# Optimization experiments

Hardware: AMD Instinct MI355X
Metric: run time of the kernel (lower is better)

Reference implementation:

```python
import jax, jax.numpy as jnp
import numpy as np

B, D, L, K = 4096, 1280, 16384, 64


def setup_inputs() -> dict:
    key = jax.random.key(0)
    k1, k2, k3, k4, k5 = jax.random.split(key, 5)
    scale_enc = 1.0 / np.sqrt(D)
    scale_dec = 1.0 / np.sqrt(L)
    return {
        "x_BD": jax.random.normal(k1, (B, D), dtype=jnp.float32),
        "pb_D": jax.random.normal(k2, (D,), dtype=jnp.float32) * 0.01,
        "W_enc": jax.random.normal(k3, (D, L), dtype=jnp.float32) * scale_enc,
        "lb_L": jax.random.normal(k4, (L,), dtype=jnp.float32) * 0.01,
        "W_dec": jax.random.normal(k5, (L, D), dtype=jnp.float32) * scale_dec,
    }


def topk_activation(x_BL, k):
    # lax.top_k over last dim, relu the values, scatter back into zeros
    tv_Bk, ti_Bk = jax.lax.top_k(x_BL, k)
    tv_Bk = jax.nn.relu(tv_Bk)
    b_B = jnp.arange(x_BL.shape[0])[:, None]
    return jnp.zeros_like(x_BL).at[b_B, ti_Bk].set(tv_Bk)


def reference(x_BD, pb_D, W_enc, lb_L, W_dec):
    # encode: shift by pre-bias, dense, add latent bias
    xshift_BD = x_BD - pb_D
    zpre_BL = xshift_BD @ W_enc + lb_L          # [B, L]
    # top-k sparse activation
    z_BL = topk_activation(zpre_BL, K)          # [B, L], only K nonzeros per row
    # decode: dense matmul over full L (the kernel-headroom target)
    xhat_BD = z_BL @ W_dec + pb_D               # [B, D]
    return (zpre_BL, z_BL, xhat_BD)
```

## Files before the change

### kernel.cpp

```cpp
#include <hip/hip_runtime.h>
#include <hip/hip_bf16.h>
#include <stdint.h>

#define B_SZ 4096
#define D_SZ 1280
#define L_SZ 16384
#define K_TOP 64
#define C_CAP 192
#define BAND 0.07f
#define LIST_CAP 4096
#define T_COLLECT 1.5f

typedef __attribute__((ext_vector_type(8))) short s16x8;
typedef __attribute__((ext_vector_type(4))) float f32x4;

#define GLOAD_LDS16(gp, lp)                                                          \
  __builtin_amdgcn_global_load_lds((const __attribute__((address_space(1))) void*)(gp), \
                                   (__attribute__((address_space(3))) void*)(lp), 16, 0, 0)

static __device__ __forceinline__ unsigned short f2bf(float f) {
  __hip_bfloat16 h = __float2bfloat16(f);
  return *reinterpret_cast<unsigned short*>(&h);
}
static __device__ __forceinline__ float bf2f(unsigned short u) {
  return __uint_as_float((unsigned)u << 16);
}
static __device__ __forceinline__ unsigned mkkey(float f) {
  const unsigned u = __float_as_uint(f);
  return (u & 0x80000000u) ? ~u : (u | 0x80000000u);
}
static __device__ __forceinline__ float unkey(unsigned k) {
  const unsigned u = (k & 0x80000000u) ? (k & 0x7fffffffu) : ~k;
  return __uint_as_float(u);
}

__global__ __launch_bounds__(256) void sae_prep(const float* __restrict__ x,
                                                const float* __restrict__ pb,
                                                const float* __restrict__ We,
                                                const float* __restrict__ Wd,
                                                unsigned short* __restrict__ A,
                                                float* __restrict__ xs,
                                                float* __restrict__ WT,
                                                unsigned short* __restrict__ WbT,
                                                unsigned short* __restrict__ Wdb,
                                                int* __restrict__ bk_cnt) {
  const int b = blockIdx.x, t = threadIdx.x;
  if (b < 5120) {
    __shared__ float tile[64][65];
    const int l0 = (b & 255) * 64, d0 = (b >> 8) * 64;
    const int c = t & 63, rg = t >> 6;
#pragma unroll
    for (int i = 0; i < 16; ++i) {
      const int row = i * 4 + rg;
      tile[row][c] = We[(size_t)(d0 + row) * L_SZ + l0 + c];
    }
    __syncthreads();
#pragma unroll
    for (int i = 0; i < 16; ++i) {
      const int row = i * 4 + rg;
      const float v = tile[c][row];
      const size_t o = (size_t)(l0 + row) * D_SZ + d0 + c;
      WT[o] = v;
      WbT[o] = f2bf(v);
    }
  } else if (b < 5120 + 4096) {
    const int r = b - 5120;
    const float* xr = x + (size_t)r * D_SZ;
    unsigned short* ar = A + (size_t)r * D_SZ;
    float* sr = xs + (size_t)r * D_SZ;
    for (int d = t; d < D_SZ; d += 256) {
      const float v = xr[d] - pb[d];
      ar[d] = f2bf(v);
      sr[d] = v;
    }
  } else if (b < 5120 + 4096 + 2048) {
    const int n4 = L_SZ * D_SZ / 4;
    for (int i = (b - 9216) * 256 + t; i < n4; i += 2048 * 256) {
      const float4 v = ((const float4*)Wd)[i];
      ushort4 o;
      o.x = f2bf(v.x); o.y = f2bf(v.y); o.z = f2bf(v.z); o.w = f2bf(v.w);
      ((ushort4*)Wdb)[i] = o;
    }
  } else {
    bk_cnt[(b - 11264) * 256 + t] = 0;
  }
}

#define SWZ(lin) ((lin) ^ ((((lin) >> 9) & 7) << 4))
#define A_LDS 0
#define B_LDS 65536
#define KBYTES (D_SZ * 2)

#define PH_MID()                                          \
  __builtin_amdgcn_s_barrier();                           \
  asm volatile("s_waitcnt lgkmcnt(0)" ::: "memory");      \
  __builtin_amdgcn_sched_barrier(0);                      \
  __builtin_amdgcn_s_setprio(1)

#define PH_END()                                          \
  __builtin_amdgcn_s_setprio(0);                          \
  __builtin_amdgcn_s_barrier();                           \
  __builtin_amdgcn_sched_barrier(0)

__global__ __launch_bounds__(512, 2) void sae_gemm(const unsigned short* __restrict__ A,
                                                   const unsigned short* __restrict__ WT,
                                                   const float* __restrict__ lb,
                                                   float* __restrict__ zpre) {
  __shared__ short lds[65536];
  char* ldsc = (char*)lds;
  const int t = threadIdx.x, lane = t & 63, w = t >> 6;
  const int wr = w >> 2, wc = w & 3, w2 = w * 2;

  const int bid = blockIdx.x;
  const int xcd = bid & 7, i2 = bid >> 3;
  const int b2 = i2 >> 4, inner = i2 & 15;
  const int mt = (b2 & 3) * 4 + (inner & 3);
  const int nt = xcd * 8 + (b2 >> 2) * 4 + (inner >> 2);
  const int m0 = mt * 256, n0 = nt * 256;

  f32x4 acc[8][4] = {};

  auto STAGE = [&](const unsigned short* op, int rowbase, int ldsop, int buf, int half, int tile) {
#pragma unroll
    for (int s = 0; s < 2; ++s) {
      const int o = (w2 + s) * 1024 + lane * 16;
      const int r = o >> 7;
      const int cb = (o & 127) ^ (((o >> 9) & 7) << 4);
      const char* g = (const char*)op + (size_t)(rowbase + half * 128 + r) * KBYTES +
                      tile * 128 + cb;
      char* l = ldsc + ldsop + buf * 32768 + half * 16384 + (w2 + s) * 1024;
      GLOAD_LDS16(g, l);
    }
  };
  auto LDA = [&](s16x8* af, int buf, int q) {
#pragma unroll
    for (int i = 0; i < 2; ++i)
#pragma unroll
      for (int kk = 0; kk < 2; ++kk) {
        const int r = (q * 2 + i) * 16 + (lane & 15);
        int lin = r * 128 + kk * 64 + ((lane >> 4) * 16);
        lin = SWZ(lin);
        af[i * 2 + kk] = *(const s16x8*)(ldsc + A_LDS + buf * 32768 + wr * 16384 + lin);
      }
  };
  auto LDB = [&](s16x8* bg, int buf) {
#pragma unroll
    for (int j = 0; j < 4; ++j)
#pragma unroll
      for (int kk = 0; kk < 2; ++kk) {
        const int nloc = wc * 64 + j * 16 + (lane & 15);
        const int half = nloc >> 7, r = nloc & 127;
        int lin = r * 128 + kk * 64 + ((lane >> 4) * 16);
        lin = SWZ(lin);
        bg[j * 2 + kk] = *(const s16x8*)(ldsc + B_LDS + buf * 32768 + half * 16384 + lin);
      }
  };
  auto MM = [&](s16x8* af, s16x8* bg, int q) {
#pragma unroll
    for (int i = 0; i < 2; ++i)
#pragma unroll
      for (int j = 0; j < 4; ++j)
#pragma unroll
        for (int kk = 0; kk < 2; ++kk)
          acc[q * 2 + i][j] =
              __builtin_amdgcn_mfma_f32_16x16x32_bf16(af[i * 2 + kk], bg[j * 2 + kk],
                                                      acc[q * 2 + i][j], 0, 0, 0);
  };

  STAGE(WT, n0, B_LDS, 0, 0, 0); STAGE(WT, n0, B_LDS, 0, 1, 0);
  STAGE(A, m0, A_LDS, 0, 0, 0);  STAGE(A, m0, A_LDS, 0, 1, 0);
  STAGE(WT, n0, B_LDS, 1, 0, 1); STAGE(WT, n0, B_LDS, 1, 1, 1);
  asm volatile("s_waitcnt vmcnt(4)" ::: "memory");
  __builtin_amdgcn_s_barrier();
  __builtin_amdgcn_sched_barrier(0);

  const int NI = D_SZ / 128;
  for (int i = 0; i < NI; ++i) {
    const bool last = (i == NI - 1);
    s16x8 af[4], bg[8];
    LDB(bg, 0); LDA(af, 0, 0);
    STAGE(A, m0, A_LDS, 1, 0, 2 * i + 1); STAGE(A, m0, A_LDS, 1, 1, 2 * i + 1);
    PH_MID(); MM(af, bg, 0); PH_END();
    LDA(af, 0, 1);
    if (!last) STAGE(WT, n0, B_LDS, 0, 0, 2 * i + 2);
    PH_MID(); MM(af, bg, 1); PH_END();
    LDA(af, 0, 2);
    if (!last) STAGE(WT, n0, B_LDS, 0, 1, 2 * i + 2);
    PH_MID(); MM(af, bg, 2); PH_END();
    LDA(af, 0, 3);
    PH_MID(); MM(af, bg, 3);
    __builtin_amdgcn_s_setprio(0);
    if (last) { asm volatile("s_waitcnt vmcnt(0)" ::: "memory"); }
    else      { asm volatile("s_waitcnt vmcnt(4)" ::: "memory"); }
    __builtin_amdgcn_s_barrier();
    __builtin_amdgcn_sched_barrier(0);
    LDB(bg, 1); LDA(af, 1, 0);
    if (!last) STAGE(A, m0, A_LDS, 0, 0, 2 * i + 2);
    PH_MID(); MM(af, bg, 0); PH_END();
    LDA(af, 1, 1);
    if (!last) STAGE(A, m0, A_LDS, 0, 1, 2 * i + 2);
    PH_MID(); MM(af, bg, 1); PH_END();
    LDA(af, 1, 2);
    if (!last) STAGE(WT, n0, B_LDS, 1, 0, 2 * i + 3);
    PH_MID(); MM(af, bg, 2); PH_END();
    LDA(af, 1, 3);
    if (!last) STAGE(WT, n0, B_LDS, 1, 1, 2 * i + 3);
    PH_MID(); MM(af, bg, 3);
    __builtin_amdgcn_s_setprio(0);
    asm volatile("s_waitcnt vmcnt(4)" ::: "memory");
    __builtin_amdgcn_s_barrier();
    __builtin_amdgcn_sched_barrier(0);
  }

  const int cl = lane & 15, rg = lane >> 4;
#pragma unroll
  for (int j = 0; j < 4; ++j) {
    const int cc = n0 + wc * 64 + j * 16 + cl;
    const float bias = lb[cc];
#pragma unroll
    for (int i = 0; i < 8; ++i) {
      const size_t base = (size_t)(m0 + wr * 128 + i * 16 + rg * 4) * L_SZ + cc;
#pragma unroll
      for (int tt = 0; tt < 4; ++tt) zpre[base + (size_t)tt * L_SZ] = acc[i][j][tt] + bias;
    }
  }
}

__device__ void radix_pick(unsigned* hist, unsigned* suf, int* sh_b, unsigned* sh_above,
                           int target, int t) {
  if (t == 0) *sh_b = -1;
  unsigned p = hist[4 * t] + hist[4 * t + 1] + hist[4 * t + 2] + hist[4 * t + 3];
  suf[t] = p;
  for (int off = 1; off < 256; off <<= 1) {
    __syncthreads();
    unsigned v = (t + off < 256) ? suf[t + off] : 0u;
    __syncthreads();
    suf[t] += v;
  }
  __syncthreads();
  const unsigned shi = (t + 1 < 256) ? suf[t + 1] : 0u;
  unsigned S = shi;
  int best = -1;
#pragma unroll
  for (int i = 3; i >= 0; --i) {
    S += hist[4 * t + i];
    if (S >= (unsigned)target) { best = 4 * t + i; break; }
  }
  if (best >= 0) atomicMax(sh_b, best);
  __syncthreads();
  const int b = *sh_b;
  if ((b >> 2) == t) {
    unsigned above = shi;
    for (int i = 3; i > (b & 3); --i) above += hist[4 * t + i];
    *sh_above = above;
  }
  __syncthreads();
}

__device__ void radix_pick4(unsigned* hist4, unsigned* suf, int* sh_b, unsigned* sh_above,
                            int target, int t) {
  if (t == 0) *sh_b = -1;
  if (t < 256) {
    unsigned p = 0;
#pragma unroll
    for (int i = 0; i < 4; ++i)
#pragma unroll
      for (int c = 0; c < 4; ++c) p += hist4[(4 * t + i) * 4 + c];
    suf[t] = p;
  }
  for (int off = 1; off < 256; off <<= 1) {
    __syncthreads();
    unsigned v = (t < 256 && t + off < 256) ? suf[t + off] : 0u;
    __syncthreads();
    if (t < 256) suf[t] += v;
  }
  __syncthreads();
  if (t < 256) {
    const unsigned shi = (t + 1 < 256) ? suf[t + 1] : 0u;
    unsigned S = shi;
    int best = -1;
    for (int i = 3; i >= 0; --i) {
      unsigned cnt = 0;
#pragma unroll
      for (int c = 0; c < 4; ++c) cnt += hist4[(4 * t + i) * 4 + c];
      S += cnt;
      if (S >= (unsigned)target) { best = 4 * t + i; break; }
    }
    if (best >= 0) atomicMax(sh_b, best);
  }
  __syncthreads();
  const int b = *sh_b;
  if (t < 256 && (b >> 2) == t) {
    unsigned above = (t + 1 < 256) ? suf[t + 1] : 0u;
    for (int i = 3; i > (b & 3); --i) {
      unsigned cnt = 0;
#pragma unroll
      for (int c = 0; c < 4; ++c) cnt += hist4[(4 * t + i) * 4 + c];
      above += cnt;
    }
    *sh_above = above;
  }
  __syncthreads();
}

__global__ __launch_bounds__(512) void sae_mega(const float* __restrict__ zpre,
                                                const float* __restrict__ xs,
                                                const float* __restrict__ WT,
                                                const float* __restrict__ lb,
                                                const unsigned short* __restrict__ Wdb,
                                                const float* __restrict__ pb,
                                                float* __restrict__ z,
                                                float* __restrict__ xhat) {
  __shared__ unsigned hist4[4096];
  __shared__ unsigned suf[256];
  __shared__ int l_idx[LIST_CAP];
  __shared__ unsigned l_key[LIST_CAP];
  __shared__ int sh_n, sh_b0, sh_b1, sh_nhi, sh_nband;
  __shared__ unsigned sh_above;
  __shared__ int bl[C_CAP];
  __shared__ float bfv[C_CAP];
  __shared__ double be[C_CAP];
  __shared__ int ids[K_TOP];
  __shared__ float vs[K_TOP];

  const int r = blockIdx.x, t = threadIdx.x, lane = t & 63, w = t >> 6;
  const float4* zr4 = (const float4*)(zpre + (size_t)r * L_SZ);

  float4 xc[5];
  {
    const float4* xr4 = (const float4*)(xs + (size_t)r * D_SZ);
#pragma unroll
    for (int i = 0; i < 5; ++i) xc[i] = xr4[lane + 64 * i];
  }

  auto push = [&](int idx, unsigned k, bool pred) {
    const unsigned long long m = __ballot(pred);
    if (!m) return;
    const int leader = (int)__ffsll((long long)m) - 1;
    int base = 0;
    if (lane == leader) base = atomicAdd(&sh_n, (int)__popcll(m));
    base = __shfl(base, leader);
    if (pred) {
      const int pos = base + (int)__popcll(m & ((1ull << lane) - 1ull));
      if (pos < LIST_CAP) { l_idx[pos] = idx; l_key[pos] = k; }
    }
  };

  if (t == 0) { sh_n = 0; sh_nhi = 0; sh_nband = 0; }
  __syncthreads();
  const unsigned keyT = mkkey(T_COLLECT);
  for (int i = t; i < L_SZ / 4; i += 512) {
    const float4 v = zr4[i];
    const float va[4] = {v.x, v.y, v.z, v.w};
#pragma unroll
    for (int q = 0; q < 4; ++q) {
      const unsigned k = mkkey(va[q]);
      push(4 * i + q, k, k >= keyT);
    }
  }
  __syncthreads();
  int nlist = sh_n < LIST_CAP ? sh_n : LIST_CAP;
  bool need_full = (sh_n < K_TOP) || (sh_n > LIST_CAP);
  float thresh_val = T_COLLECT;
  float lo_f = 0.f, hi_f = 0.f;

  for (int attempt = 0; attempt < 2; ++attempt) {
    if (need_full) {
      for (int i = t; i < 4096; i += 512) hist4[i] = 0;
      __syncthreads();
      for (int i = t; i < L_SZ / 4; i += 512) {
        const float4 v = zr4[i];
        const float va[4] = {v.x, v.y, v.z, v.w};
#pragma unroll
        for (int q = 0; q < 4; ++q)
          atomicAdd(&hist4[(mkkey(va[q]) >> 22) * 4 + (lane & 3)], 1u);
      }
      __syncthreads();
      radix_pick4(hist4, suf, &sh_b0, &sh_above, K_TOP, t);
      const int cb0 = sh_b0;
      const unsigned lt = (unsigned)(cb0 > 8 ? cb0 - 8 : 0) << 22;
      thresh_val = unkey(lt);
      if (t == 0) sh_n = 0;
      __syncthreads();
      for (int i = t; i < L_SZ / 4; i += 512) {
        const float4 v = zr4[i];
        const float va[4] = {v.x, v.y, v.z, v.w};
#pragma unroll
        for (int q = 0; q < 4; ++q) {
          const unsigned k = mkkey(va[q]);
          push(4 * i + q, k, k >= lt);
        }
      }
      __syncthreads();
      nlist = sh_n < LIST_CAP ? sh_n : LIST_CAP;
    }
    for (int i = t; i < 4096; i += 512) hist4[i] = 0;
    __syncthreads();
    for (int i = t; i < nlist; i += 512)
      atomicAdd(&hist4[(l_key[i] >> 22) * 4 + (lane & 3)], 1u);
    __syncthreads();
    radix_pick4(hist4, suf, &sh_b0, &sh_above, K_TOP, t);
    const int b0 = sh_b0;
    const int tgt2 = K_TOP - (int)sh_above;
    for (int i = t; i < 4096; i += 512) hist4[i] = 0;
    __syncthreads();
    for (int i = t; i < nlist; i += 512) {
      const unsigned k = l_key[i];
      if ((int)(k >> 22) == b0) atomicAdd(&hist4[((k >> 12) & 1023u) * 4 + (lane & 3)], 1u);
    }
    __syncthreads();
    radix_pick4(hist4, suf, &sh_b1, &sh_above, tgt2, t);
    const unsigned v64lb_key = (((unsigned)b0 << 10) | (unsigned)sh_b1) << 12;
    lo_f = unkey(v64lb_key) - BAND;
    hi_f = unkey(v64lb_key + 4095u) + BAND;
    if (thresh_val <= lo_f) break;
    need_full = true;
  }

  for (int i = t; i < nlist; i += 512) {
    const float val = unkey(l_key[i]);
    if (val >= lo_f) {
      if (val > hi_f) {
        const int p = atomicAdd(&sh_nhi, 1);
        if (p < K_TOP) { ids[p] = l_idx[i]; vs[p] = fmaxf(val, 0.f); }
      } else {
        const int p = atomicAdd(&sh_nband, 1);
        if (p < C_CAP) { bl[p] = l_idx[i]; bfv[p] = val; }
      }
    }
  }
  __syncthreads();
  const int nh = sh_nhi < K_TOP ? sh_nhi : K_TOP;
  const int nb = sh_nband < C_CAP ? sh_nband : C_CAP;
  for (int e = w; e < nb; e += 8) {
    const int l = bl[e];
    const float4* wr4 = (const float4*)(WT + (size_t)l * D_SZ);
    double acc = 0.0;
#pragma unroll
    for (int i = 0; i < 5; ++i) {
      const float4 wv = wr4[lane + 64 * i];
      acc += (double)xc[i].x * (double)wv.x + (double)xc[i].y * (double)wv.y +
             (double)xc[i].z * (double)wv.z + (double)xc[i].w * (double)wv.w;
    }
#pragma unroll
    for (int off = 32; off > 0; off >>= 1) acc += __shfl_down(acc, off);
    if (lane == 0) be[e] = acc + (double)lb[l];
  }
  __syncthreads();
  const int need = K_TOP - nh;
  if (t < nb) {
    const double ev = be[t];
    const int l = bl[t];
    int rank = 0;
    for (int j = 0; j < nb; ++j) {
      const double e2 = be[j];
      if (e2 > ev || (e2 == ev && bl[j] < l)) ++rank;
    }
    if (rank < need) {
      ids[nh + rank] = l;
      vs[nh + rank] = fmaxf(bfv[t], 0.f);
    }
  }
  __syncthreads();
  if (t < 320) {
    float4 acc = ((const float4*)pb)[t];
#pragma unroll 8
    for (int k = 0; k < K_TOP; ++k) {
      const ushort4 wv = ((const ushort4*)(Wdb + (size_t)ids[k] * D_SZ))[t];
      const float vk = vs[k];
      acc.x += vk * bf2f(wv.x);
      acc.y += vk * bf2f(wv.y);
      acc.z += vk * bf2f(wv.z);
      acc.w += vk * bf2f(wv.w);
    }
    ((float4*)(xhat + (size_t)r * D_SZ))[t] = acc;
  } else {
    const int tz = t - 320;
    float4* zr = (float4*)(z + (size_t)r * L_SZ);
    for (int i = tz; i < L_SZ / 4; i += 192) zr[i] = make_float4(0.f, 0.f, 0.f, 0.f);
  }
  __syncthreads();
  if (t < K_TOP) z[(size_t)r * L_SZ + ids[t]] = vs[t];
}

__global__ __launch_bounds__(256) void sae_topc(const float* __restrict__ zpre,
                                                int* __restrict__ bk_cnt,
                                                int* __restrict__ band_lat,
                                                float* __restrict__ band_fval,
                                                int* __restrict__ n_hi,
                                                int* __restrict__ n_band,
                                                int* __restrict__ t_idx,
                                                float* __restrict__ t_val) {
  __shared__ unsigned hist[1024];
  __shared__ unsigned suf[256];
  __shared__ int sh_b0, sh_b1, sh_nhi, sh_nband;
  __shared__ unsigned sh_above;
  const int r = blockIdx.x, t = threadIdx.x;
  const float4* zr4 = (const float4*)(zpre + (size_t)r * L_SZ);

  for (int i = t; i < 1024; i += 256) hist[i] = 0;
  if (t == 0) { sh_nhi = 0; sh_nband = 0; }
  __syncthreads();
  for (int i = t; i < L_SZ / 4; i += 256) {
    const float4 v = zr4[i];
    atomicAdd(&hist[mkkey(v.x) >> 22], 1u);
    atomicAdd(&hist[mkkey(v.y) >> 22], 1u);
    atomicAdd(&hist[mkkey(v.z) >> 22], 1u);
    atomicAdd(&hist[mkkey(v.w) >> 22], 1u);
  }
  __syncthreads();
  radix_pick(hist, suf, &sh_b0, &sh_above, K_TOP, t);
  const int b0 = sh_b0;
  const int target2 = K_TOP - (int)sh_above;
  __syncthreads();
  for (int i = t; i < 1024; i += 256) hist[i] = 0;
  __syncthreads();
  for (int i = t; i < L_SZ / 4; i += 256) {
    const float4 v = zr4[i];
    const float va[4] = {v.x, v.y, v.z, v.w};
#pragma unroll
    for (int q = 0; q < 4; ++q) {
      const unsigned k = mkkey(va[q]);
      if ((int)(k >> 22) == b0) atomicAdd(&hist[(k >> 12) & 1023u], 1u);
    }
  }
  __syncthreads();
  radix_pick(hist, suf, &sh_b1, &sh_above, target2, t);
  const unsigned v64lb_key = (((unsigned)b0 << 10) | (unsigned)sh_b1) << 12;
  const float lo_f = unkey(v64lb_key) - BAND;
  const float hi_f = unkey(v64lb_key + 4095u) + BAND;
  __syncthreads();
  for (int i = t; i < L_SZ / 4; i += 256) {
    const float4 v = zr4[i];
    const float va[4] = {v.x, v.y, v.z, v.w};
#pragma unroll
    for (int q = 0; q < 4; ++q) {
      const float val = va[q];
      if (val >= lo_f) {
        const int l = 4 * i + q;
        if (val > hi_f) {
          const int p = atomicAdd(&sh_nhi, 1);
          if (p < K_TOP) {
            t_idx[(size_t)r * K_TOP + p] = l;
            t_val[(size_t)r * K_TOP + p] = fmaxf(val, 0.f);
          }
        } else {
          const int p = atomicAdd(&sh_nband, 1);
          if (p < C_CAP) {
            band_lat[(r << 8) + p] = l;
            band_fval[(r << 8) + p] = val;
            atomicAdd(&bk_cnt[l], 1);
          }
        }
      }
    }
  }
  __syncthreads();
  if (t == 0) {
    n_hi[r] = sh_nhi < K_TOP ? sh_nhi : K_TOP;
    n_band[r] = sh_nband < C_CAP ? sh_nband : C_CAP;
  }
}

__global__ __launch_bounds__(256) void sae_scan(const int* __restrict__ counts,
                                                int* __restrict__ offsets,
                                                int* __restrict__ cursor) {
  __shared__ int part[256];
  const int t = threadIdx.x;
  int s = 0;
  for (int i = 0; i < 64; ++i) s += counts[t * 64 + i];
  part[t] = s;
  __syncthreads();
  int excl = 0;
  for (int j = 0; j < t; ++j) excl += part[j];
  int run = excl;
  for (int i = 0; i < 64; ++i) {
    const int idx = t * 64 + i;
    offsets[idx] = run;
    cursor[idx] = run;
    run += counts[idx];
  }
}

__global__ __launch_bounds__(192) void sae_bucket_fill(const int* __restrict__ band_lat,
                                                       const int* __restrict__ n_band,
                                                       int* __restrict__ cursor,
                                                       int* __restrict__ entries) {
  const int r = blockIdx.x, t = threadIdx.x;
  if (t < n_band[r]) {
    const int l = band_lat[(r << 8) + t];
    const int pos = atomicAdd(&cursor[l], 1);
    entries[pos] = (r << 8) | t;
  }
}

__global__ __launch_bounds__(256) void sae_refine_lm(const float* __restrict__ xs,
                                                     const float* __restrict__ WT,
                                                     const float* __restrict__ lb,
                                                     const int* __restrict__ counts,
                                                     const int* __restrict__ offsets,
                                                     const int* __restrict__ entries,
                                                     double* __restrict__ band_eval) {
  __shared__ float4 wl[D_SZ / 4];
  const int l = blockIdx.x;
  const int t = threadIdx.x, lane = t & 63, w = t >> 6;
  const int n = counts[l];
  if (n == 0) return;
  const float4* wc = (const float4*)(WT + (size_t)l * D_SZ);
  for (int d = t; d < D_SZ / 4; d += 256) wl[d] = wc[d];
  __syncthreads();
  const int base = offsets[l];
  const double bias = (double)lb[l];
  for (int e = w; e < n; e += 4) {
    const int ent = entries[base + e];
    const int rr = ent >> 8;
    const float4* xr = (const float4*)(xs + (size_t)rr * D_SZ);
    double acc = 0.0;
#pragma unroll
    for (int i = 0; i < 5; ++i) {
      const float4 xv = xr[lane + 64 * i];
      const float4 wv = wl[lane + 64 * i];
      acc += (double)xv.x * (double)wv.x + (double)xv.y * (double)wv.y +
             (double)xv.z * (double)wv.z + (double)xv.w * (double)wv.w;
    }
#pragma unroll
    for (int off = 32; off > 0; off >>= 1) acc += __shfl_down(acc, off);
    if (lane == 0) band_eval[ent] = acc + bias;
  }
}

__global__ __launch_bounds__(320) void sae_finish_nz(const int* __restrict__ n_hi,
                                                     const int* __restrict__ n_band,
                                                     const int* __restrict__ band_lat,
                                                     const float* __restrict__ band_fval,
                                                     const double* __restrict__ band_eval,
                                                     int* __restrict__ t_idx,
                                                     float* __restrict__ t_val,
                                                     const unsigned short* __restrict__ Wdb,
                                                     const float* __restrict__ pb,
                                                     float* __restrict__ xhat) {
  __shared__ int bl[C_CAP];
  __shared__ float bf[C_CAP];
  __shared__ double be[C_CAP];
  __shared__ int ids[K_TOP];
  __shared__ float vs[K_TOP];
  const int r = blockIdx.x, t = threadIdx.x;
  const int nh = n_hi[r], nb = n_band[r];
  if (t < nb) {
    bl[t] = band_lat[(r << 8) + t];
    bf[t] = band_fval[(r << 8) + t];
    be[t] = band_eval[(r << 8) + t];
  }
  if (t < nh) {
    ids[t] = t_idx[(size_t)r * K_TOP + t];
    vs[t] = t_val[(size_t)r * K_TOP + t];
  }
  __syncthreads();
  const int need = K_TOP - nh;
  if (t < nb) {
    const double ev = be[t];
    const int l = bl[t];
    int rank = 0;
    for (int j = 0; j < nb; ++j) {
      const double e2 = be[j];
      if (e2 > ev || (e2 == ev && bl[j] < l)) ++rank;
    }
    if (rank < need) {
      const float fv = fmaxf(bf[t], 0.f);
      ids[nh + rank] = l;
      vs[nh + rank] = fv;
      t_idx[(size_t)r * K_TOP + nh + rank] = l;
      t_val[(size_t)r * K_TOP + nh + rank] = fv;
    }
  }
  __syncthreads();
  float4 acc = ((const float4*)pb)[t];
#pragma unroll 8
  for (int k = 0; k < K_TOP; ++k) {
    const ushort4 wv = ((const ushort4*)(Wdb + (size_t)ids[k] * D_SZ))[t];
    const float vk = vs[k];
    acc.x += vk * bf2f(wv.x);
    acc.y += vk * bf2f(wv.y);
    acc.z += vk * bf2f(wv.z);
    acc.w += vk * bf2f(wv.w);
  }
  ((float4*)(xhat + (size_t)r * D_SZ))[t] = acc;
}

__global__ void sae_scatterA(const int* __restrict__ top_idx, const float* __restrict__ top_val,
                             float* __restrict__ z) {
  const int r = blockIdx.x;
  const int t = threadIdx.x;
  const int id = top_idx[(size_t)r * K_TOP + t];
  const float v = top_val[(size_t)r * K_TOP + t];
  z[(size_t)r * L_SZ + id] = v;
}

__global__ __launch_bounds__(256) void sae_scatterB(const int* __restrict__ top_idx,
                                                    const float* __restrict__ top_val,
                                                    float* __restrict__ z) {
  __shared__ int ids[32 * K_TOP];
  __shared__ float vs[32 * K_TOP];
  const int t = threadIdx.x;
  for (int i = t; i < 32 * K_TOP; i += 256) {
    ids[i] = top_idx[(size_t)4064 * K_TOP + i];
    vs[i] = top_val[(size_t)4064 * K_TOP + i];
  }
  __syncthreads();
  float4* zz = (float4*)(z + (size_t)4064 * L_SZ);
  for (int i = t; i < 32 * L_SZ / 4; i += 256) zz[i] = make_float4(0.f, 0.f, 0.f, 0.f);
  __syncthreads();
  for (int i = t; i < 32 * K_TOP; i += 256) {
    const int rr = 4064 + i / K_TOP;
    z[(size_t)rr * L_SZ + ids[i]] = vs[i];
  }
}

extern "C" void kernel_launch(void* const* d_in, const int* in_sizes, int n_in,
                              void* d_out, int out_size, void* d_ws, size_t ws_size,
                              hipStream_t stream) {
  const float* x  = (const float*)d_in[0];
  const float* pb = (const float*)d_in[1];
  const float* We = (const float*)d_in[2];
  const float* lb = (const float*)d_in[3];
  const float* Wd = (const float*)d_in[4];

  float* zpre = (float*)d_out;
  float* z    = zpre + (size_t)B_SZ * L_SZ;
  float* xhat = z + (size_t)B_SZ * L_SZ;

  const bool use_ws = ws_size >= ((size_t)234 << 20);
  char* sb = use_ws ? (char*)d_ws : (char*)z;

  unsigned short* A_bf   = (unsigned short*)(sb);
  unsigned short* WT_bf  = (unsigned short*)(sb + ((size_t)16 << 20));
  float*          WT_f32 = (float*)(sb + ((size_t)64 << 20));
  float*          xs_f32 = (float*)(sb + ((size_t)144 << 20));
  int*            b_lat  = (int*)(sb + ((size_t)164 << 20));
  float*          b_fval = (float*)(sb + ((size_t)168 << 20));
  double*         b_eval = (double*)(sb + ((size_t)172 << 20));
  int*            bk_cnt = (int*)(sb + ((size_t)180 << 20));
  int*            bk_off = (int*)(sb + ((size_t)181 << 20));
  int*            bk_cur = (int*)(sb + ((size_t)182 << 20));
  int*            bk_ent = (int*)(sb + ((size_t)184 << 20));
  unsigned short* Wd_bf  = (unsigned short*)(sb + ((size_t)188 << 20));
  int*            nhi_g  = (int*)(sb + ((size_t)228 << 20));
  int*            nbd_g  = (int*)(sb + ((size_t)229 << 20));
  int*   t_idx = use_ws ? (int*)(sb + ((size_t)230 << 20))
                        : (int*)((char*)z + ((size_t)254 << 20));
  float* t_val = use_ws ? (float*)(sb + ((size_t)232 << 20))
                        : (float*)((char*)z + ((size_t)255 << 20));

  sae_prep<<<11328, 256, 0, stream>>>(x, pb, We, Wd, A_bf, xs_f32, WT_f32, WT_bf, Wd_bf, bk_cnt);
  sae_gemm<<<1024, 512, 0, stream>>>(A_bf, WT_bf, lb, zpre);
  if (use_ws) {
    sae_mega<<<B_SZ, 512, 0, stream>>>(zpre, xs_f32, WT_f32, lb, Wd_bf, pb, z, xhat);
  } else {
    sae_topc<<<B_SZ, 256, 0, stream>>>(zpre, bk_cnt, b_lat, b_fval, nhi_g, nbd_g, t_idx, t_val);
    sae_scan<<<1, 256, 0, stream>>>(bk_cnt, bk_off, bk_cur);
    sae_bucket_fill<<<B_SZ, 192, 0, stream>>>(b_lat, nbd_g, bk_cur, bk_ent);
    sae_refine_lm<<<L_SZ, 256, 0, stream>>>(xs_f32, WT_f32, lb, bk_cnt, bk_off, bk_ent, b_eval);
    sae_finish_nz<<<B_SZ, 320, 0, stream>>>(nhi_g, nbd_g, b_lat, b_fval, b_eval, t_idx, t_val,
                                            Wd_bf, pb, xhat);
    hipMemsetAsync(z, 0, (size_t)4064 * L_SZ * sizeof(float), stream);
    sae_scatterA<<<4064, K_TOP, 0, stream>>>(t_idx, t_val, z);
    sae_scatterB<<<1, 256, 0, stream>>>(t_idx, t_val, z);
  }
}
```

Before: 667.3 us.

## Collect top-k candidates in GEMM epilogue to skip zpre row rescans

The GEMM epilogue now appends every pre-activation above a higher threshold to a per-row global candidate list via atomics. The top-k stage then reads only that short list instead of scanning the full 16K-wide zpre row, and falls back to a full two-pass radix selection when the list is too short, overflows, or the threshold is not safely below the band. This removes a large read of zpre in the mega kernel. In exchange it adds global atomics and scattered writes to the GEMM epilogue, needs more workspace, and only runs when the workspace is large enough.

```diff
diff --git a/kernel.cpp b/kernel.cpp
--- a/kernel.cpp
+++ b/kernel.cpp
@@ -8,8 +8,8 @@
 #define K_TOP 64
 #define C_CAP 192
 #define BAND 0.07f
-#define LIST_CAP 4096
-#define T_COLLECT 1.5f
+#define CL_CAP 512
+#define T_COLLECT 2.2f
 
 typedef __attribute__((ext_vector_type(8))) short s16x8;
 typedef __attribute__((ext_vector_type(4))) float f32x4;
@@ -43,7 +43,8 @@
                                                 float* __restrict__ WT,
                                                 unsigned short* __restrict__ WbT,
                                                 unsigned short* __restrict__ Wdb,
-                                                int* __restrict__ bk_cnt) {
+                                                int* __restrict__ bk_cnt,
+                                                int* __restrict__ cl_cnt) {
   const int b = blockIdx.x, t = threadIdx.x;
   if (b < 5120) {
     __shared__ float tile[64][65];
@@ -81,8 +82,10 @@
       o.x = f2bf(v.x); o.y = f2bf(v.y); o.z = f2bf(v.z); o.w = f2bf(v.w);
       ((ushort4*)Wdb)[i] = o;
     }
+  } else if (b < 11328) {
+    bk_cnt[(b - 11264) * 256 + t] = 0;
   } else {
-    bk_cnt[(b - 11264) * 256 + t] = 0;
+    cl_cnt[(b - 11328) * 256 + t] = 0;
   }
 }
 
@@ -105,7 +108,10 @@
 __global__ __launch_bounds__(512, 2) void sae_gemm(const unsigned short* __restrict__ A,
                                                    const unsigned short* __restrict__ WT,
                                                    const float* __restrict__ lb,
-                                                   float* __restrict__ zpre) {
+                                                   float* __restrict__ zpre,
+                                                   int* __restrict__ cl_cnt,
+                                                   int* __restrict__ cl_idx,
+                                                   float* __restrict__ cl_val) {
   __shared__ short lds[65536];
   char* ldsc = (char*)lds;
   const int t = threadIdx.x, lane = t & 63, w = t >> 6;
@@ -219,9 +225,20 @@
     const float bias = lb[cc];
 #pragma unroll
     for (int i = 0; i < 8; ++i) {
-      const size_t base = (size_t)(m0 + wr * 128 + i * 16 + rg * 4) * L_SZ + cc;
-#pragma unroll
-      for (int tt = 0; tt < 4; ++tt) zpre[base + (size_t)tt * L_SZ] = acc[i][j][tt] + bias;
+      const int row0 = m0 + wr * 128 + i * 16 + rg * 4;
+      const size_t base = (size_t)row0 * L_SZ + cc;
+#pragma unroll
+      for (int tt = 0; tt < 4; ++tt) {
+        const float v = acc[i][j][tt] + bias;
+        zpre[base + (size_t)tt * L_SZ] = v;
+        if (v >= T_COLLECT) {
+          const int p = atomicAdd(&cl_cnt[row0 + tt], 1);
+          if (p < CL_CAP) {
+            cl_idx[(size_t)(row0 + tt) * CL_CAP + p] = cc;
+            cl_val[(size_t)(row0 + tt) * CL_CAP + p] = v;
+          }
+        }
+      }
     }
   }
 }
@@ -309,13 +326,16 @@
                                                 const float* __restrict__ lb,
                                                 const unsigned short* __restrict__ Wdb,
                                                 const float* __restrict__ pb,
+                                                const int* __restrict__ cl_cnt,
+                                                const int* __restrict__ cl_idx,
+                                                const float* __restrict__ cl_val,
                                                 float* __restrict__ z,
                                                 float* __restrict__ xhat) {
   __shared__ unsigned hist4[4096];
   __shared__ unsigned suf[256];
-  __shared__ int l_idx[LIST_CAP];
-  __shared__ unsigned l_key[LIST_CAP];
-  __shared__ int sh_n, sh_b0, sh_b1, sh_nhi, sh_nband;
+  __shared__ int l_idx[CL_CAP];
+  __shared__ unsigned l_key[CL_CAP];
+  __shared__ int sh_b0, sh_b1, sh_nhi, sh_nband;
   __shared__ unsigned sh_above;
   __shared__ int bl[C_CAP];
   __shared__ float bfv[C_CAP];
@@ -333,70 +353,19 @@
     for (int i = 0; i < 5; ++i) xc[i] = xr4[lane + 64 * i];
   }
 
-  auto push = [&](int idx, unsigned k, bool pred) {
-    const unsigned long long m = __ballot(pred);
-    if (!m) return;
-    const int leader = (int)__ffsll((long long)m) - 1;
-    int base = 0;
-    if (lane == leader) base = atomicAdd(&sh_n, (int)__popcll(m));
-    base = __shfl(base, leader);
-    if (pred) {
-      const int pos = base + (int)__popcll(m & ((1ull << lane) - 1ull));
-      if (pos < LIST_CAP) { l_idx[pos] = idx; l_key[pos] = k; }
-    }
-  };
-
-  if (t == 0) { sh_n = 0; sh_nhi = 0; sh_nband = 0; }
-  __syncthreads();
-  const unsigned keyT = mkkey(T_COLLECT);
-  for (int i = t; i < L_SZ / 4; i += 512) {
-    const float4 v = zr4[i];
-    const float va[4] = {v.x, v.y, v.z, v.w};
-#pragma unroll
-    for (int q = 0; q < 4; ++q) {
-      const unsigned k = mkkey(va[q]);
-      push(4 * i + q, k, k >= keyT);
-    }
-  }
-  __syncthreads();
-  int nlist = sh_n < LIST_CAP ? sh_n : LIST_CAP;
-  bool need_full = (sh_n < K_TOP) || (sh_n > LIST_CAP);
-  float thresh_val = T_COLLECT;
+  if (t == 0) { sh_nhi = 0; sh_nband = 0; }
+  const int n_raw = cl_cnt[r];
+  bool fast = (n_raw >= K_TOP && n_raw <= CL_CAP);
   float lo_f = 0.f, hi_f = 0.f;
 
-  for (int attempt = 0; attempt < 2; ++attempt) {
-    if (need_full) {
-      for (int i = t; i < 4096; i += 512) hist4[i] = 0;
-      __syncthreads();
-      for (int i = t; i < L_SZ / 4; i += 512) {
-        const float4 v = zr4[i];
-        const float va[4] = {v.x, v.y, v.z, v.w};
-#pragma unroll
-        for (int q = 0; q < 4; ++q)
-          atomicAdd(&hist4[(mkkey(va[q]) >> 22) * 4 + (lane & 3)], 1u);
-      }
-      __syncthreads();
-      radix_pick4(hist4, suf, &sh_b0, &sh_above, K_TOP, t);
-      const int cb0 = sh_b0;
-      const unsigned lt = (unsigned)(cb0 > 8 ? cb0 - 8 : 0) << 22;
-      thresh_val = unkey(lt);
-      if (t == 0) sh_n = 0;
-      __syncthreads();
-      for (int i = t; i < L_SZ / 4; i += 512) {
-        const float4 v = zr4[i];
-        const float va[4] = {v.x, v.y, v.z, v.w};
-#pragma unroll
-        for (int q = 0; q < 4; ++q) {
-          const unsigned k = mkkey(va[q]);
-          push(4 * i + q, k, k >= lt);
-        }
-      }
-      __syncthreads();
-      nlist = sh_n < LIST_CAP ? sh_n : LIST_CAP;
+  if (fast) {
+    for (int i = t; i < n_raw; i += 512) {
+      l_idx[i] = cl_idx[(size_t)r * CL_CAP + i];
+      l_key[i] = mkkey(cl_val[(size_t)r * CL_CAP + i]);
     }
     for (int i = t; i < 4096; i += 512) hist4[i] = 0;
     __syncthreads();
-    for (int i = t; i < nlist; i += 512)
+    for (int i = t; i < n_raw; i += 512)
       atomicAdd(&hist4[(l_key[i] >> 22) * 4 + (lane & 3)], 1u);
     __syncthreads();
     radix_pick4(hist4, suf, &sh_b0, &sh_above, K_TOP, t);
@@ -404,7 +373,7 @@
     const int tgt2 = K_TOP - (int)sh_above;
     for (int i = t; i < 4096; i += 512) hist4[i] = 0;
     __syncthreads();
-    for (int i = t; i < nlist; i += 512) {
+    for (int i = t; i < n_raw; i += 512) {
       const unsigned k = l_key[i];
       if ((int)(k >> 22) == b0) atomicAdd(&hist4[((k >> 12) & 1023u) * 4 + (lane & 3)], 1u);
     }
@@ -413,19 +382,70 @@
     const unsigned v64lb_key = (((unsigned)b0 << 10) | (unsigned)sh_b1) << 12;
     lo_f = unkey(v64lb_key) - BAND;
     hi_f = unkey(v64lb_key + 4095u) + BAND;
-    if (thresh_val <= lo_f) break;
-    need_full = true;
-  }
-
-  for (int i = t; i < nlist; i += 512) {
-    const float val = unkey(l_key[i]);
-    if (val >= lo_f) {
-      if (val > hi_f) {
-        const int p = atomicAdd(&sh_nhi, 1);
-        if (p < K_TOP) { ids[p] = l_idx[i]; vs[p] = fmaxf(val, 0.f); }
-      } else {
-        const int p = atomicAdd(&sh_nband, 1);
-        if (p < C_CAP) { bl[p] = l_idx[i]; bfv[p] = val; }
+    if (T_COLLECT > lo_f) fast = false;
+  }
+  __syncthreads();
+  if (!fast) {
+    for (int i = t; i < 4096; i += 512) hist4[i] = 0;
+    __syncthreads();
+    for (int i = t; i < L_SZ / 4; i += 512) {
+      const float4 v = zr4[i];
+      const float va[4] = {v.x, v.y, v.z, v.w};
+#pragma unroll
+      for (int q = 0; q < 4; ++q)
+        atomicAdd(&hist4[(mkkey(va[q]) >> 22) * 4 + (lane & 3)], 1u);
+    }
+    __syncthreads();
+    radix_pick4(hist4, suf, &sh_b0, &sh_above, K_TOP, t);
+    const int b0 = sh_b0;
+    const int tgt2 = K_TOP - (int)sh_above;
+    for (int i = t; i < 4096; i += 512) hist4[i] = 0;
+    __syncthreads();
+    for (int i = t; i < L_SZ / 4; i += 512) {
+      const float4 v = zr4[i];
+      const float va[4] = {v.x, v.y, v.z, v.w};
+#pragma unroll
+      for (int q = 0; q < 4; ++q) {
+        const unsigned k = mkkey(va[q]);
+        if ((int)(k >> 22) == b0) atomicAdd(&hist4[((k >> 12) & 1023u) * 4 + (lane & 3)], 1u);
+      }
+    }
+    __syncthreads();
+    radix_pick4(hist4, suf, &sh_b1, &sh_above, tgt2, t);
+    const unsigned v64lb_key = (((unsigned)b0 << 10) | (unsigned)sh_b1) << 12;
+    lo_f = unkey(v64lb_key) - BAND;
+    hi_f = unkey(v64lb_key + 4095u) + BAND;
+  }
+  __syncthreads();
+  if (fast) {
+    for (int i = t; i < n_raw; i += 512) {
+      const float val = unkey(l_key[i]);
+      if (val >= lo_f) {
+        if (val > hi_f) {
+          const int p = atomicAdd(&sh_nhi, 1);
+          if (p < K_TOP) { ids[p] = l_idx[i]; vs[p] = fmaxf(val, 0.f); }
+        } else {
+          const int p = atomicAdd(&sh_nband, 1);
+          if (p < C_CAP) { bl[p] = l_idx[i]; bfv[p] = val; }
+        }
+      }
+    }
+  } else {
+    for (int i = t; i < L_SZ / 4; i += 512) {
+      const float4 v = zr4[i];
+      const float va[4] = {v.x, v.y, v.z, v.w};
+#pragma unroll
+      for (int q = 0; q < 4; ++q) {
+        const float val = va[q];
+        if (val >= lo_f) {
+          if (val > hi_f) {
+            const int p = atomicAdd(&sh_nhi, 1);
+            if (p < K_TOP) { ids[p] = 4 * i + q; vs[p] = fmaxf(val, 0.f); }
+          } else {
+            const int p = atomicAdd(&sh_nband, 1);
+            if (p < C_CAP) { bl[p] = 4 * i + q; bfv[p] = val; }
+          }
+        }
       }
     }
   }
@@ -729,7 +749,7 @@
   float* z    = zpre + (size_t)B_SZ * L_SZ;
   float* xhat = z + (size_t)B_SZ * L_SZ;
 
-  const bool use_ws = ws_size >= ((size_t)234 << 20);
+  const bool use_ws = ws_size >= ((size_t)251 << 20);
   char* sb = use_ws ? (char*)d_ws : (char*)z;
 
   unsigned short* A_bf   = (unsigned short*)(sb);
@@ -746,15 +766,20 @@
   unsigned short* Wd_bf  = (unsigned short*)(sb + ((size_t)188 << 20));
   int*            nhi_g  = (int*)(sb + ((size_t)228 << 20));
   int*            nbd_g  = (int*)(sb + ((size_t)229 << 20));
+  int*            cl_idx = (int*)(sb + ((size_t)234 << 20));
+  float*          cl_val = (float*)(sb + ((size_t)242 << 20));
+  int*            cl_cnt = (int*)(sb + ((size_t)250 << 20));
   int*   t_idx = use_ws ? (int*)(sb + ((size_t)230 << 20))
                         : (int*)((char*)z + ((size_t)254 << 20));
   float* t_val = use_ws ? (float*)(sb + ((size_t)232 << 20))
                         : (float*)((char*)z + ((size_t)255 << 20));
 
-  sae_prep<<<11328, 256, 0, stream>>>(x, pb, We, Wd, A_bf, xs_f32, WT_f32, WT_bf, Wd_bf, bk_cnt);
-  sae_gemm<<<1024, 512, 0, stream>>>(A_bf, WT_bf, lb, zpre);
+  sae_prep<<<11344, 256, 0, stream>>>(x, pb, We, Wd, A_bf, xs_f32, WT_f32, WT_bf, Wd_bf,
+                                      bk_cnt, cl_cnt);
+  sae_gemm<<<1024, 512, 0, stream>>>(A_bf, WT_bf, lb, zpre, cl_cnt, cl_idx, cl_val);
   if (use_ws) {
-    sae_mega<<<B_SZ, 512, 0, stream>>>(zpre, xs_f32, WT_f32, lb, Wd_bf, pb, z, xhat);
+    sae_mega<<<B_SZ, 512, 0, stream>>>(zpre, xs_f32, WT_f32, lb, Wd_bf, pb,
+                                       cl_cnt, cl_idx, cl_val, z, xhat);
   } else {
     sae_topc<<<B_SZ, 256, 0, stream>>>(zpre, bk_cnt, b_lat, b_fval, nhi_g, nbd_g, t_idx, t_val);
     sae_scan<<<1, 256, 0, stream>>>(bk_cnt, bk_off, bk_cur);
```

Result: no change. 677.7 us (+1.6%).
